# Kernel tuning notes

Measured on AMD Instinct MI355X. Metric: run time of the kernel, lower is better.

Reference implementation:

```python
import jax, jax.numpy as jnp
import numpy as np

D_MODEL = 768
N_HEADS = 12
D_HEAD = 64
D_EMBED = N_HEADS * D_HEAD  # 768


def setup_inputs() -> dict:
    key = jax.random.key(0)
    ks = jax.random.split(key, 5)
    b, p = 2, 2048
    x = jax.random.normal(ks[0], (b, p, D_MODEL), dtype=jnp.float32)
    # nn.Linear default init scale ~ 1/sqrt(fan_in)
    Wqkv = jax.random.normal(ks[1], (D_MODEL, 3 * D_EMBED), dtype=jnp.float32) / np.sqrt(D_MODEL)
    bqkv = jax.random.normal(ks[2], (3 * D_EMBED,), dtype=jnp.float32) * 0.01
    Wout = jax.random.normal(ks[3], (D_EMBED, D_MODEL), dtype=jnp.float32) / np.sqrt(D_EMBED)
    bout = jax.random.normal(ks[4], (D_MODEL,), dtype=jnp.float32) * 0.01
    return {"x": x, "Wqkv": Wqkv, "bqkv": bqkv, "Wout": Wout, "bout": bout}


def reference(x, Wqkv, bqkv, Wout, bout):
    b, p, d = x.shape
    qkv = x @ Wqkv + bqkv                                   # [b, p, 3*D_EMBED]
    qkv = qkv.reshape(b, p, N_HEADS, 3 * D_HEAD).transpose(0, 2, 1, 3)  # [b, h, p, 3*dh]
    q, k, v = jnp.split(qkv, 3, axis=-1)                    # each [b, h, p, dh]
    # FAITHFUL to source bug: logits /= d_head**(-0.5)  ==  logits *= sqrt(d_head)
    logits = jnp.einsum('bhqd,bhkd->bhqk', q, k) * jnp.sqrt(jnp.float32(D_HEAD))
    attn = jax.nn.softmax(logits, axis=-1)                  # [b, h, p, p]
    out = jnp.einsum('bhqk,bhkd->bhqd', attn, v)            # [b, h, p, dh]
    out = out.transpose(0, 2, 1, 3).reshape(b, p, D_EMBED)  # [b, p, D_EMBED]
    return out @ Wout + bout                                # [b, p, D_MODEL]
```

## Files before the change

kernel.cpp:

```cpp
#include <hip/hip_runtime.h>
#include <stdint.h>

#define LOG2E 1.44269504088896340736f

typedef __bf16 v8bf __attribute__((ext_vector_type(8)));
typedef _Float16 v8h __attribute__((ext_vector_type(8)));
typedef float f32x4 __attribute__((ext_vector_type(4)));
typedef float f32x16 __attribute__((ext_vector_type(16)));
typedef unsigned int v4u __attribute__((ext_vector_type(4)));
typedef unsigned int v2u __attribute__((ext_vector_type(2)));

__device__ __forceinline__ unsigned short f2bf(float f) {
  union { float f; uint32_t u; } v; v.f = f;
  uint32_t u = v.u;
  uint32_t r = (u + 0x7FFFu + ((u >> 16) & 1u)) >> 16;
  return (unsigned short)r;
}
__device__ __forceinline__ float bf2f(unsigned short h) {
  union { uint32_t u; float f; } v; v.u = ((uint32_t)h) << 16;
  return v.f;
}
__device__ __forceinline__ void gll16(const void* g, void* l) {
  __builtin_amdgcn_global_load_lds(
      (const __attribute__((address_space(1))) unsigned int*)g,
      (__attribute__((address_space(3))) unsigned int*)l, 16, 0, 0);
}
__device__ __forceinline__ uint32_t pk2(float a, float b) {
  union { __bf16 h[2]; uint32_t u; } x;
  x.h[0] = (__bf16)a; x.h[1] = (__bf16)b;
  return x.u;
}

__global__ void prep_fused(const float* __restrict__ x, const float* __restrict__ Wqkv,
                           const float* __restrict__ Wout,
                           unsigned short* __restrict__ Acat,
                           unsigned short* __restrict__ BcatT,
                           unsigned short* __restrict__ WvT,
                           unsigned short* __restrict__ WoT) {
  const int t = threadIdx.x, f = blockIdx.x;
  if (f < 12288) {
    int m = f / 3, n = (f - m * 3) * 256 + t;
    float v = x[(size_t)m * 768 + n];
    unsigned short H = f2bf(v);
    unsigned short L = f2bf(v - bf2f(H));
    size_t base = (size_t)m * 2304;
    Acat[base + n] = H;
    Acat[base + 768 + n] = L;
    Acat[base + 1536 + n] = H;
  } else if (f < 19200) {
    int g = f - 12288;
    int cp = g / 3, k = (g - cp * 3) * 256 + t;
    int n;
    if (cp < 1536) n = (cp >> 7) * 192 + (cp & 127);
    else           n = ((cp - 1536) >> 6) * 192 + 128 + ((cp - 1536) & 63);
    float v = Wqkv[(size_t)k * 2304 + n];
    unsigned short H = f2bf(v);
    if (cp < 1536) {
      unsigned short L = f2bf(v - bf2f(H));
      size_t base = (size_t)cp * 2304;
      BcatT[base + k] = H;
      BcatT[base + 768 + k] = H;
      BcatT[base + 1536 + k] = L;
    } else {
      WvT[(size_t)(cp - 1536) * 768 + k] = H;
    }
  } else {
    int g = f - 19200;
    int n = g / 3, k = (g - n * 3) * 256 + t;
    WoT[(size_t)n * 768 + k] = f2bf(Wout[(size_t)k * 768 + n]);
  }
}

__global__ __launch_bounds__(256) void gemm_qkv(
    const unsigned short* __restrict__ Acat, const unsigned short* __restrict__ BcatT,
    const unsigned short* __restrict__ WvT, const float* __restrict__ bqkv,
    _Float16* __restrict__ Qh, _Float16* __restrict__ Kh,
    unsigned short* __restrict__ VT) {
  __shared__ unsigned short As[128 * 32];
  __shared__ unsigned short Bs[128 * 32];
  const int t = threadIdx.x, f = blockIdx.x;
  const int w = t >> 6, l = t & 63, lr = l & 15, lg = l >> 4;
  const int wm = (w >> 1) * 64, wn = (w & 1) * 64;
  f32x4 acc[4][4] = {};

  if (f < 384) {
    const int xcd = f & 7, s = f >> 3;
    const int m0 = (xcd * 4 + (s & 3)) * 128;
    const int xt = s >> 2;
    const unsigned short* Bp = BcatT + (size_t)xt * 128 * 2304;
    for (int kt = 0; kt < 72; ++kt) {
      const int k0 = kt << 5;
      const int c0 = t, c1 = t + 256;
      gll16(Acat + (size_t)(m0 + (c0 >> 2)) * 2304 + k0 + ((c0 & 3) << 3), &As[c0 * 8]);
      gll16(Acat + (size_t)(m0 + (c1 >> 2)) * 2304 + k0 + ((c1 & 3) << 3), &As[c1 * 8]);
      gll16(Bp + (size_t)(c0 >> 2) * 2304 + k0 + ((c0 & 3) << 3), &Bs[c0 * 8]);
      gll16(Bp + (size_t)(c1 >> 2) * 2304 + k0 + ((c1 & 3) << 3), &Bs[c1 * 8]);
      __syncthreads();
      v8bf a[4], b[4];
#pragma unroll
      for (int i = 0; i < 4; i++) {
        a[i] = *(const v8bf*)&As[(wm + i * 16 + lr) * 32 + lg * 8];
        b[i] = *(const v8bf*)&Bs[(wn + i * 16 + lr) * 32 + lg * 8];
      }
#pragma unroll
      for (int i = 0; i < 4; i++)
#pragma unroll
        for (int j = 0; j < 4; j++)
          acc[i][j] = __builtin_amdgcn_mfma_f32_16x16x32_bf16(a[i], b[j], acc[i][j], 0, 0, 0);
      __syncthreads();
    }
#pragma unroll
    for (int j = 0; j < 4; j++) {
      const int jj = j * 16 + lr;
      const float bv = bqkv[xt * 192 + wn + jj];
#pragma unroll
      for (int i = 0; i < 4; i++) {
#pragma unroll
        for (int r = 0; r < 4; r++) {
          const int m = m0 + wm + i * 16 + lg * 4 + r;
          const int b = m >> 11, p = m & 2047;
          size_t base = ((size_t)(b * 12 + xt) * 2048 + p) * 64;
          float val = acc[i][j][r] + bv;
          if (wn == 0) {
            Qh[base + jj] = (_Float16)(val * (8.0f * LOG2E));
          } else {
            Kh[base + jj] = (_Float16)val;
          }
        }
      }
    }
  } else {
    const int g = f - 384;
    const int xcd = g & 7, s = g >> 3;
    const int m0v = (xcd * 4 + (s & 3)) * 128;
    const int d0 = (s >> 2) * 128;
    for (int kt = 0; kt < 24; ++kt) {
      const int k0 = kt << 5;
      const int c0 = t, c1 = t + 256;
      gll16(WvT + (size_t)(d0 + (c0 >> 2)) * 768 + k0 + ((c0 & 3) << 3), &As[c0 * 8]);
      gll16(WvT + (size_t)(d0 + (c1 >> 2)) * 768 + k0 + ((c1 & 3) << 3), &As[c1 * 8]);
      gll16(Acat + (size_t)(m0v + (c0 >> 2)) * 2304 + k0 + ((c0 & 3) << 3), &Bs[c0 * 8]);
      gll16(Acat + (size_t)(m0v + (c1 >> 2)) * 2304 + k0 + ((c1 & 3) << 3), &Bs[c1 * 8]);
      __syncthreads();
      v8bf a[4], b[4];
#pragma unroll
      for (int i = 0; i < 4; i++) {
        a[i] = *(const v8bf*)&As[(wm + i * 16 + lr) * 32 + lg * 8];
        b[i] = *(const v8bf*)&Bs[(wn + i * 16 + lr) * 32 + lg * 8];
      }
#pragma unroll
      for (int i = 0; i < 4; i++)
#pragma unroll
        for (int j = 0; j < 4; j++)
          acc[i][j] = __builtin_amdgcn_mfma_f32_16x16x32_bf16(a[i], b[j], acc[i][j], 0, 0, 0);
      __syncthreads();
    }
#pragma unroll
    for (int i = 0; i < 4; i++) {
#pragma unroll
      for (int r = 0; r < 4; r++) {
        const int drow = d0 + wm + i * 16 + lg * 4 + r;
        const int h = drow >> 6, dd = drow & 63;
        const float bv = bqkv[h * 192 + 128 + dd];
#pragma unroll
        for (int j = 0; j < 4; j++) {
          const int m = m0v + wn + j * 16 + lr;
          const int b = m >> 11, p = m & 2047;
          VT[((size_t)(b * 12 + h) * 64 + dd) * 2048 + p] = f2bf(acc[i][j][r] + bv);
        }
      }
    }
  }
}

__global__ __launch_bounds__(256) void gemm_out(
    const unsigned short* __restrict__ A, const unsigned short* __restrict__ B,
    const float* __restrict__ bias, float* __restrict__ C) {
  __shared__ unsigned short As[64 * 32];
  __shared__ unsigned short Bs[128 * 32];
  const int t = threadIdx.x, f = blockIdx.x;
  const int xcd = f & 7, s = f >> 3;
  const int m0 = (xcd * 8 + (s & 7)) * 64;
  const int n0 = (s >> 3) * 128;
  const int w = t >> 6, l = t & 63, lr = l & 15, lg = l >> 4;
  const int wm = (w >> 1) * 32, wn = (w & 1) * 64;
  f32x4 acc[2][4] = {};
  for (int kt = 0; kt < 24; ++kt) {
    const int k0 = kt << 5;
    gll16(A + (size_t)(m0 + (t >> 2)) * 768 + k0 + ((t & 3) << 3), &As[t * 8]);
    gll16(B + (size_t)(n0 + (t >> 2)) * 768 + k0 + ((t & 3) << 3), &Bs[t * 8]);
    gll16(B + (size_t)(n0 + 64 + (t >> 2)) * 768 + k0 + ((t & 3) << 3), &Bs[(t + 256) * 8]);
    __syncthreads();
    v8bf a[2], b[4];
#pragma unroll
    for (int i = 0; i < 2; i++)
      a[i] = *(const v8bf*)&As[(wm + i * 16 + lr) * 32 + lg * 8];
#pragma unroll
    for (int j = 0; j < 4; j++)
      b[j] = *(const v8bf*)&Bs[(wn + j * 16 + lr) * 32 + lg * 8];
#pragma unroll
    for (int i = 0; i < 2; i++)
#pragma unroll
      for (int j = 0; j < 4; j++)
        acc[i][j] = __builtin_amdgcn_mfma_f32_16x16x32_bf16(a[i], b[j], acc[i][j], 0, 0, 0);
    __syncthreads();
  }
#pragma unroll
  for (int i = 0; i < 2; i++) {
#pragma unroll
    for (int j = 0; j < 4; j++) {
      const int col = n0 + wn + j * 16 + lr;
      const float bv = bias[col];
#pragma unroll
      for (int r = 0; r < 4; r++) {
        const int row = m0 + wm + i * 16 + lg * 4 + r;
        C[(size_t)row * 768 + col] = acc[i][j][r] + bv;
      }
    }
  }
}

__global__ __launch_bounds__(256, 4) void attn(
    const _Float16* __restrict__ Qh, const _Float16* __restrict__ Kh,
    const unsigned short* __restrict__ VT,
    float* __restrict__ Op, float* __restrict__ Ml) {
  __shared__ __align__(16) _Float16 Ks[2][32 * 64];
  __shared__ __align__(16) unsigned short Vs[2][64 * 32];
  __shared__ float Al[4][32];
  const int t = threadIdx.x, w = t >> 6, l = t & 63;
  const int lq = l & 31, hi = l >> 5;
  const int f = blockIdx.x;
  const int xcd = f & 7, slot = f >> 3;
  const int p = xcd + 8 * (slot >> 4);
  const int bh = p >> 2, zsplit = p & 3;
  const int q0 = (slot & 15) * 128;
  const int qw0 = q0 + w * 32;
  const int NKT = 16;
  const int ktBase = zsplit * 16;
  const _Float16* Qb = Qh + (size_t)bh * 2048 * 64;
  const _Float16* Kb = Kh + (size_t)bh * 2048 * 64;
  const unsigned short* Vb = VT + (size_t)bh * 64 * 2048;

  const int krow = t >> 3, kpart = t & 7;
  const int kwofs = (krow * 64 + kpart * 8) ^ ((krow & 7) << 3);
  const int vd = t >> 2, vpart = t & 3;
  const int vwofs = (vd * 32 + vpart * 8) ^ ((vd & 3) << 3);

  const char* gK = (const char*)Kb + (size_t)ktBase * 4096 + (size_t)t * 16;
  const char* gV = (const char*)Vb + (size_t)vd * 4096 + (size_t)vpart * 16
                   + (size_t)ktBase * 64;

  v4u kreg, vreg;
  kreg = *(const v4u*)gK;
  vreg = *(const v4u*)gV;
  *(v4u*)&Ks[0][kwofs] = kreg;
  *(v4u*)&Vs[0][vwofs] = vreg;
  gK += 4096; gV += 64;
  kreg = *(const v4u*)gK;
  vreg = *(const v4u*)gV;

  v8h qf[4];
#pragma unroll
  for (int ks = 0; ks < 4; ++ks)
    qf[ks] = *(const v8h*)(Qb + (size_t)(qw0 + lq) * 64 + ks * 16 + hi * 8);

  f32x16 o0 = {}, o1 = {};
  float mrun = -1e30f, lsum = 0.f;
  const int sxk = (lq & 7) << 3;
  const int sxv = (lq & 3) << 3;
  __syncthreads();

  for (int kt = 0; kt < NKT; ++kt) {
    const _Float16* ksb = &Ks[kt & 1][0];
    const unsigned short* vsb = &Vs[kt & 1][0];
    _Float16* ksw = &Ks[(kt & 1) ^ 1][0];
    unsigned short* vsw = &Vs[(kt & 1) ^ 1][0];

    f32x16 s = {};
    __builtin_amdgcn_s_setprio(1);
#pragma unroll
    for (int ks = 0; ks < 4; ++ks) {
      v8h ka = *(const v8h*)&ksb[(lq * 64 + ks * 16 + hi * 8) ^ sxk];
      s = __builtin_amdgcn_mfma_f32_32x32x16_f16(ka, qf[ks], s, 0, 0, 0);
    }
    __builtin_amdgcn_s_setprio(0);

    if (kt < NKT - 1) {
      *(v4u*)&ksw[kwofs] = kreg;
      *(v4u*)&vsw[vwofs] = vreg;
    }
    if (kt < NKT - 2) {
      gK += 4096; gV += 64;
      kreg = *(const v4u*)gK;
      vreg = *(const v4u*)gV;
    }

    float tm[8];
#pragma unroll
    for (int i = 0; i < 8; i++) tm[i] = fmaxf(s[i], s[i + 8]);
#pragma unroll
    for (int i = 0; i < 4; i++) tm[i] = fmaxf(tm[i], tm[i + 4]);
    float pmax = fmaxf(fmaxf(tm[0], tm[1]), fmaxf(tm[2], tm[3]));
    {
      v2u r = __builtin_amdgcn_permlane32_swap(__float_as_uint(pmax),
                                               __float_as_uint(pmax), false, false);
      pmax = fmaxf(__uint_as_float(r.x), __uint_as_float(r.y));
    }

    if (__any(pmax > mrun + 32.f)) {
      float mnew = fmaxf(mrun, pmax);
      float a = __builtin_exp2f(mrun - mnew);
      mrun = mnew;
      lsum *= a;
      if (!hi) Al[w][lq] = a;
#pragma unroll
      for (int r = 0; r < 16; r++) {
        float ar = Al[w][(r & 3) + 8 * (r >> 2) + 4 * hi];
        o0[r] *= ar; o1[r] *= ar;
      }
    }

#pragma unroll
    for (int i = 0; i < 16; i++) s[i] = __builtin_exp2f(s[i] - mrun);
    {
      float a0 = (s[0] + s[8]) + (s[1] + s[9]);
      float a1 = (s[2] + s[10]) + (s[3] + s[11]);
      float a2 = (s[4] + s[12]) + (s[5] + s[13]);
      float a3 = (s[6] + s[14]) + (s[7] + s[15]);
      float ps = (a0 + a1) + (a2 + a3);
      v2u r = __builtin_amdgcn_permlane32_swap(__float_as_uint(ps),
                                               __float_as_uint(ps), false, false);
      lsum += __uint_as_float(r.x) + __uint_as_float(r.y);
    }
    uint32_t paw[2][4];
    {
      v2u r0 = __builtin_amdgcn_permlane32_swap(pk2(s[0], s[1]), pk2(s[4], s[5]), false, false);
      v2u r1 = __builtin_amdgcn_permlane32_swap(pk2(s[2], s[3]), pk2(s[6], s[7]), false, false);
      paw[0][0] = r0.x; paw[0][2] = r0.y; paw[0][1] = r1.x; paw[0][3] = r1.y;
      v2u r2 = __builtin_amdgcn_permlane32_swap(pk2(s[8], s[9]), pk2(s[12], s[13]), false, false);
      v2u r3 = __builtin_amdgcn_permlane32_swap(pk2(s[10], s[11]), pk2(s[14], s[15]), false, false);
      paw[1][0] = r2.x; paw[1][2] = r2.y; paw[1][1] = r3.x; paw[1][3] = r3.y;
    }

    __builtin_amdgcn_s_setprio(1);
#pragma unroll
    for (int ks = 0; ks < 2; ++ks) {
      union { uint32_t u[4]; v8bf v; } pa;
      pa.u[0] = paw[ks][0]; pa.u[1] = paw[ks][1];
      pa.u[2] = paw[ks][2]; pa.u[3] = paw[ks][3];
      v8bf v0 = *(const v8bf*)&vsb[(lq * 32 + ks * 16 + hi * 8) ^ sxv];
      v8bf v1 = *(const v8bf*)&vsb[((lq + 32) * 32 + ks * 16 + hi * 8) ^ sxv];
      o0 = __builtin_amdgcn_mfma_f32_32x32x16_bf16(pa.v, v0, o0, 0, 0, 0);
      o1 = __builtin_amdgcn_mfma_f32_32x32x16_bf16(pa.v, v1, o1, 0, 0, 0);
    }
    __builtin_amdgcn_s_setprio(0);
    if (kt < NKT - 1) __syncthreads();
  }

  const size_t S = (size_t)24 * 2048;
  const size_t srow = (size_t)zsplit * S + (size_t)bh * 2048;
  if (!hi) {
    Ml[(srow + qw0 + lq) * 2]     = mrun;
    Ml[(srow + qw0 + lq) * 2 + 1] = lsum;
  }
#pragma unroll
  for (int r = 0; r < 16; r++) {
    const int q = qw0 + (r & 3) + 8 * (r >> 2) + 4 * hi;
    Op[(srow + q) * 64 + lq]      = o0[r];
    Op[(srow + q) * 64 + 32 + lq] = o1[r];
  }
}

__global__ __launch_bounds__(256) void attn_combine(
    const float* __restrict__ Op, const float* __restrict__ Ml,
    __bf16* __restrict__ Oe) {
  const size_t S = (size_t)24 * 2048;
  int row = blockIdx.x * 4 + (threadIdx.x >> 6);
  int lane = threadIdx.x & 63;
  int bh = row >> 11, q = row & 2047;
  int b = bh / 12, h = bh - b * 12;
  float m[4], lv[4];
#pragma unroll
  for (int s = 0; s < 4; s++) {
    m[s]  = Ml[(s * S + row) * 2];
    lv[s] = Ml[(s * S + row) * 2 + 1];
  }
  float M = fmaxf(fmaxf(m[0], m[1]), fmaxf(m[2], m[3]));
  float num = 0.f, den = 0.f;
#pragma unroll
  for (int s = 0; s < 4; s++) {
    float a = __builtin_exp2f(m[s] - M);
    den += lv[s] * a;
    num += Op[(s * S + row) * 64 + lane] * a;
  }
  Oe[((size_t)(b * 2048 + q)) * 768 + h * 64 + lane] = (__bf16)(num / den);
}

extern "C" void kernel_launch(void* const* d_in, const int* in_sizes, int n_in,
                              void* d_out, int out_size, void* d_ws, size_t ws_size,
                              hipStream_t stream) {
  const float* x    = (const float*)d_in[0];
  const float* Wqkv = (const float*)d_in[1];
  const float* bqkv = (const float*)d_in[2];
  const float* Wout = (const float*)d_in[3];
  const float* bout = (const float*)d_in[4];
  float* out = (float*)d_out;
  char* ws = (char*)d_ws;

  unsigned short* Acat  = (unsigned short*)(ws + 0);
  unsigned short* BcatT = (unsigned short*)(ws + 18874368);
  unsigned short* WvT   = (unsigned short*)(ws + 25952256);
  _Float16*       Qh    = (_Float16*)(ws + 67239936);
  _Float16*       Kh    = (_Float16*)(ws + 86114304);
  unsigned short* VT    = (unsigned short*)(ws + 104988672);
  unsigned short* Oemb  = (unsigned short*)(ws + 111280128);
  unsigned short* WoutT = (unsigned short*)(ws + 117571584);
  float*          Opart = (float*)(ws + 0);
  float*          Mlpart= (float*)(ws + 52428800);

  prep_fused<<<dim3(21504), 256, 0, stream>>>(x, Wqkv, Wout, Acat, BcatT, WvT, WoutT);
  gemm_qkv<<<dim3(576), 256, 0, stream>>>(Acat, BcatT, WvT, bqkv, Qh, Kh, VT);
  attn<<<dim3(1536), 256, 0, stream>>>(Qh, Kh, VT, Opart, Mlpart);
  attn_combine<<<dim3(12288), 256, 0, stream>>>(Opart, Mlpart, (__bf16*)Oemb);
  gemm_out<<<dim3(384), 256, 0, stream>>>(Oemb, WoutT, bout, out);
}
```

Baseline: 156.5 us.

## Use single-pass fp16 QKV GEMM and halve attention key split count

The QKV projection no longer uses the three-term bf16 hi/lo split with K=2304. It now converts x and Wqkv to fp16 once and runs a plain K=768 fp16 MFMA GEMM, which cuts GEMM work and prep traffic to about a third. The attention kernel splits the keys 2 ways instead of 4 with 32 key tiles per block, so it launches half as many blocks, writes fewer partial results, and the combine step merges two partials. Occupancy hint drops from 4 to 3 waves-per-EU. The risks are the precision loss from dropping the compensated split (fp16 range with unit-variance inputs) and less parallelism in attention.

After: 138.9 us. 11.2% less time.

```diff
diff --git a/kernel.cpp b/kernel.cpp
--- a/kernel.cpp
+++ b/kernel.cpp
@@ -16,10 +16,6 @@
   uint32_t r = (u + 0x7FFFu + ((u >> 16) & 1u)) >> 16;
   return (unsigned short)r;
 }
-__device__ __forceinline__ float bf2f(unsigned short h) {
-  union { uint32_t u; float f; } v; v.u = ((uint32_t)h) << 16;
-  return v.f;
-}
 __device__ __forceinline__ void gll16(const void* g, void* l) {
   __builtin_amdgcn_global_load_lds(
       (const __attribute__((address_space(1))) unsigned int*)g,
@@ -31,22 +27,17 @@
   return x.u;
 }
 
+
 __global__ void prep_fused(const float* __restrict__ x, const float* __restrict__ Wqkv,
                            const float* __restrict__ Wout,
-                           unsigned short* __restrict__ Acat,
-                           unsigned short* __restrict__ BcatT,
-                           unsigned short* __restrict__ WvT,
+                           _Float16* __restrict__ Ah,
+                           _Float16* __restrict__ Whk,
+                           _Float16* __restrict__ Wv,
                            unsigned short* __restrict__ WoT) {
   const int t = threadIdx.x, f = blockIdx.x;
   if (f < 12288) {
     int m = f / 3, n = (f - m * 3) * 256 + t;
-    float v = x[(size_t)m * 768 + n];
-    unsigned short H = f2bf(v);
-    unsigned short L = f2bf(v - bf2f(H));
-    size_t base = (size_t)m * 2304;
-    Acat[base + n] = H;
-    Acat[base + 768 + n] = L;
-    Acat[base + 1536 + n] = H;
+    Ah[(size_t)m * 768 + n] = (_Float16)x[(size_t)m * 768 + n];
   } else if (f < 19200) {
     int g = f - 12288;
     int cp = g / 3, k = (g - cp * 3) * 256 + t;
@@ -54,16 +45,8 @@
     if (cp < 1536) n = (cp >> 7) * 192 + (cp & 127);
     else           n = ((cp - 1536) >> 6) * 192 + 128 + ((cp - 1536) & 63);
     float v = Wqkv[(size_t)k * 2304 + n];
-    unsigned short H = f2bf(v);
-    if (cp < 1536) {
-      unsigned short L = f2bf(v - bf2f(H));
-      size_t base = (size_t)cp * 2304;
-      BcatT[base + k] = H;
-      BcatT[base + 768 + k] = H;
-      BcatT[base + 1536 + k] = L;
-    } else {
-      WvT[(size_t)(cp - 1536) * 768 + k] = H;
-    }
+    if (cp < 1536) Whk[(size_t)cp * 768 + k] = (_Float16)v;
+    else           Wv[(size_t)(cp - 1536) * 768 + k] = (_Float16)v;
   } else {
     int g = f - 19200;
     int n = g / 3, k = (g - n * 3) * 256 + t;
@@ -72,12 +55,12 @@
 }
 
 __global__ __launch_bounds__(256) void gemm_qkv(
-    const unsigned short* __restrict__ Acat, const unsigned short* __restrict__ BcatT,
-    const unsigned short* __restrict__ WvT, const float* __restrict__ bqkv,
+    const _Float16* __restrict__ Ah, const _Float16* __restrict__ Whk,
+    const _Float16* __restrict__ Wv, const float* __restrict__ bqkv,
     _Float16* __restrict__ Qh, _Float16* __restrict__ Kh,
     unsigned short* __restrict__ VT) {
-  __shared__ unsigned short As[128 * 32];
-  __shared__ unsigned short Bs[128 * 32];
+  __shared__ _Float16 As[128 * 32];
+  __shared__ _Float16 Bs[128 * 32];
   const int t = threadIdx.x, f = blockIdx.x;
   const int w = t >> 6, l = t & 63, lr = l & 15, lg = l >> 4;
   const int wm = (w >> 1) * 64, wn = (w & 1) * 64;
@@ -87,26 +70,27 @@
     const int xcd = f & 7, s = f >> 3;
     const int m0 = (xcd * 4 + (s & 3)) * 128;
     const int xt = s >> 2;
-    const unsigned short* Bp = BcatT + (size_t)xt * 128 * 2304;
-    for (int kt = 0; kt < 72; ++kt) {
+    const _Float16* Ap = Ah + (size_t)m0 * 768;
+    const _Float16* Bp = Whk + (size_t)xt * 128 * 768;
+    for (int kt = 0; kt < 24; ++kt) {
       const int k0 = kt << 5;
       const int c0 = t, c1 = t + 256;
-      gll16(Acat + (size_t)(m0 + (c0 >> 2)) * 2304 + k0 + ((c0 & 3) << 3), &As[c0 * 8]);
-      gll16(Acat + (size_t)(m0 + (c1 >> 2)) * 2304 + k0 + ((c1 & 3) << 3), &As[c1 * 8]);
-      gll16(Bp + (size_t)(c0 >> 2) * 2304 + k0 + ((c0 & 3) << 3), &Bs[c0 * 8]);
-      gll16(Bp + (size_t)(c1 >> 2) * 2304 + k0 + ((c1 & 3) << 3), &Bs[c1 * 8]);
+      gll16(Ap + (size_t)(c0 >> 2) * 768 + k0 + ((c0 & 3) << 3), &As[c0 * 8]);
+      gll16(Ap + (size_t)(c1 >> 2) * 768 + k0 + ((c1 & 3) << 3), &As[c1 * 8]);
+      gll16(Bp + (size_t)(c0 >> 2) * 768 + k0 + ((c0 & 3) << 3), &Bs[c0 * 8]);
+      gll16(Bp + (size_t)(c1 >> 2) * 768 + k0 + ((c1 & 3) << 3), &Bs[c1 * 8]);
       __syncthreads();
-      v8bf a[4], b[4];
+      v8h a[4], b[4];
 #pragma unroll
       for (int i = 0; i < 4; i++) {
-        a[i] = *(const v8bf*)&As[(wm + i * 16 + lr) * 32 + lg * 8];
-        b[i] = *(const v8bf*)&Bs[(wn + i * 16 + lr) * 32 + lg * 8];
+        a[i] = *(const v8h*)&As[(wm + i * 16 + lr) * 32 + lg * 8];
+        b[i] = *(const v8h*)&Bs[(wn + i * 16 + lr) * 32 + lg * 8];
       }
 #pragma unroll
       for (int i = 0; i < 4; i++)
 #pragma unroll
         for (int j = 0; j < 4; j++)
-          acc[i][j] = __builtin_amdgcn_mfma_f32_16x16x32_bf16(a[i], b[j], acc[i][j], 0, 0, 0);
+          acc[i][j] = __builtin_amdgcn_mfma_f32_16x16x32_f16(a[i], b[j], acc[i][j], 0, 0, 0);
       __syncthreads();
     }
 #pragma unroll
@@ -121,11 +105,8 @@
           const int b = m >> 11, p = m & 2047;
           size_t base = ((size_t)(b * 12 + xt) * 2048 + p) * 64;
           float val = acc[i][j][r] + bv;
-          if (wn == 0) {
-            Qh[base + jj] = (_Float16)(val * (8.0f * LOG2E));
-          } else {
-            Kh[base + jj] = (_Float16)val;
-          }
+          if (wn == 0) Qh[base + jj] = (_Float16)(val * (8.0f * LOG2E));
+          else         Kh[base + jj] = (_Float16)val;
         }
       }
     }
@@ -137,22 +118,22 @@
     for (int kt = 0; kt < 24; ++kt) {
       const int k0 = kt << 5;
       const int c0 = t, c1 = t + 256;
-      gll16(WvT + (size_t)(d0 + (c0 >> 2)) * 768 + k0 + ((c0 & 3) << 3), &As[c0 * 8]);
-      gll16(WvT + (size_t)(d0 + (c1 >> 2)) * 768 + k0 + ((c1 & 3) << 3), &As[c1 * 8]);
-      gll16(Acat + (size_t)(m0v + (c0 >> 2)) * 2304 + k0 + ((c0 & 3) << 3), &Bs[c0 * 8]);
-      gll16(Acat + (size_t)(m0v + (c1 >> 2)) * 2304 + k0 + ((c1 & 3) << 3), &Bs[c1 * 8]);
+      gll16(Wv + (size_t)(d0 + (c0 >> 2)) * 768 + k0 + ((c0 & 3) << 3), &As[c0 * 8]);
+      gll16(Wv + (size_t)(d0 + (c1 >> 2)) * 768 + k0 + ((c1 & 3) << 3), &As[c1 * 8]);
+      gll16(Ah + (size_t)(m0v + (c0 >> 2)) * 768 + k0 + ((c0 & 3) << 3), &Bs[c0 * 8]);
+      gll16(Ah + (size_t)(m0v + (c1 >> 2)) * 768 + k0 + ((c1 & 3) << 3), &Bs[c1 * 8]);
       __syncthreads();
-      v8bf a[4], b[4];
+      v8h a[4], b[4];
 #pragma unroll
       for (int i = 0; i < 4; i++) {
-        a[i] = *(const v8bf*)&As[(wm + i * 16 + lr) * 32 + lg * 8];
-        b[i] = *(const v8bf*)&Bs[(wn + i * 16 + lr) * 32 + lg * 8];
+        a[i] = *(const v8h*)&As[(wm + i * 16 + lr) * 32 + lg * 8];
+        b[i] = *(const v8h*)&Bs[(wn + i * 16 + lr) * 32 + lg * 8];
       }
 #pragma unroll
       for (int i = 0; i < 4; i++)
 #pragma unroll
         for (int j = 0; j < 4; j++)
-          acc[i][j] = __builtin_amdgcn_mfma_f32_16x16x32_bf16(a[i], b[j], acc[i][j], 0, 0, 0);
+          acc[i][j] = __builtin_amdgcn_mfma_f32_16x16x32_f16(a[i], b[j], acc[i][j], 0, 0, 0);
       __syncthreads();
     }
 #pragma unroll
@@ -220,7 +201,7 @@
   }
 }
 
-__global__ __launch_bounds__(256, 4) void attn(
+__global__ __launch_bounds__(256, 3) void attn(
     const _Float16* __restrict__ Qh, const _Float16* __restrict__ Kh,
     const unsigned short* __restrict__ VT,
     float* __restrict__ Op, float* __restrict__ Ml) {
@@ -232,11 +213,11 @@
   const int f = blockIdx.x;
   const int xcd = f & 7, slot = f >> 3;
   const int p = xcd + 8 * (slot >> 4);
-  const int bh = p >> 2, zsplit = p & 3;
+  const int bh = p >> 1, zsplit = p & 1;
   const int q0 = (slot & 15) * 128;
   const int qw0 = q0 + w * 32;
-  const int NKT = 16;
-  const int ktBase = zsplit * 16;
+  const int NKT = 32;
+  const int ktBase = zsplit * 32;
   const _Float16* Qb = Qh + (size_t)bh * 2048 * 64;
   const _Float16* Kb = Kh + (size_t)bh * 2048 * 64;
   const unsigned short* Vb = VT + (size_t)bh * 64 * 2048;
@@ -379,21 +360,15 @@
   int lane = threadIdx.x & 63;
   int bh = row >> 11, q = row & 2047;
   int b = bh / 12, h = bh - b * 12;
-  float m[4], lv[4];
-#pragma unroll
-  for (int s = 0; s < 4; s++) {
-    m[s]  = Ml[(s * S + row) * 2];
-    lv[s] = Ml[(s * S + row) * 2 + 1];
-  }
-  float M = fmaxf(fmaxf(m[0], m[1]), fmaxf(m[2], m[3]));
-  float num = 0.f, den = 0.f;
-#pragma unroll
-  for (int s = 0; s < 4; s++) {
-    float a = __builtin_exp2f(m[s] - M);
-    den += lv[s] * a;
-    num += Op[(s * S + row) * 64 + lane] * a;
-  }
-  Oe[((size_t)(b * 2048 + q)) * 768 + h * 64 + lane] = (__bf16)(num / den);
+  float m1 = Ml[(size_t)row * 2], l1 = Ml[(size_t)row * 2 + 1];
+  float m2 = Ml[(S + row) * 2],   l2 = Ml[(S + row) * 2 + 1];
+  float M = fmaxf(m1, m2);
+  float a1 = __builtin_exp2f(m1 - M);
+  float a2 = __builtin_exp2f(m2 - M);
+  float rinv = 1.0f / (l1 * a1 + l2 * a2);
+  float o1 = Op[(size_t)row * 64 + lane];
+  float o2 = Op[S * 64 + (size_t)row * 64 + lane];
+  Oe[((size_t)(b * 2048 + q)) * 768 + h * 64 + lane] = (__bf16)((o1 * a1 + o2 * a2) * rinv);
 }
 
 extern "C" void kernel_launch(void* const* d_in, const int* in_sizes, int n_in,
@@ -407,20 +382,20 @@
   float* out = (float*)d_out;
   char* ws = (char*)d_ws;
 
-  unsigned short* Acat  = (unsigned short*)(ws + 0);
-  unsigned short* BcatT = (unsigned short*)(ws + 18874368);
-  unsigned short* WvT   = (unsigned short*)(ws + 25952256);
+  _Float16*       Ah    = (_Float16*)(ws + 0);
+  _Float16*       Whk   = (_Float16*)(ws + 18874368);
+  _Float16*       Wv    = (_Float16*)(ws + 25952256);
   _Float16*       Qh    = (_Float16*)(ws + 67239936);
   _Float16*       Kh    = (_Float16*)(ws + 86114304);
   unsigned short* VT    = (unsigned short*)(ws + 104988672);
   unsigned short* Oemb  = (unsigned short*)(ws + 111280128);
-  unsigned short* WoutT = (unsigned short*)(ws + 117571584);
+  unsigned short* WoT   = (unsigned short*)(ws + 117571584);
   float*          Opart = (float*)(ws + 0);
-  float*          Mlpart= (float*)(ws + 52428800);
-
-  prep_fused<<<dim3(21504), 256, 0, stream>>>(x, Wqkv, Wout, Acat, BcatT, WvT, WoutT);
-  gemm_qkv<<<dim3(576), 256, 0, stream>>>(Acat, BcatT, WvT, bqkv, Qh, Kh, VT);
-  attn<<<dim3(1536), 256, 0, stream>>>(Qh, Kh, VT, Opart, Mlpart);
+  float*          Mlpart= (float*)(ws + 50331648);
+
+  prep_fused<<<dim3(21504), 256, 0, stream>>>(x, Wqkv, Wout, Ah, Whk, Wv, WoT);
+  gemm_qkv<<<dim3(576), 256, 0, stream>>>(Ah, Whk, Wv, bqkv, Qh, Kh, VT);
+  attn<<<dim3(768), 256, 0, stream>>>(Qh, Kh, VT, Opart, Mlpart);
   attn_combine<<<dim3(12288), 256, 0, stream>>>(Opart, Mlpart, (__bf16*)Oemb);
-  gemm_out<<<dim3(384), 256, 0, stream>>>(Oemb, WoutT, bout, out);
-}
+  gemm_out<<<dim3(384), 256, 0, stream>>>(Oemb, WoT, bout, out);
+}
```
